# Kernel tuning notes

Hardware: AMD Instinct MI355X
Metric: run time of the kernel (lower is better)

## Reference

```python
import jax, jax.numpy as jnp
import numpy as np

N_NODES = 30000
N_EDGES = 480000
N_GRAPHS = 128
D_IN = 128
D_H = 256
N_CLASSES = 60


def gcn_conv(x, src, dst, norm, W, b, num_nodes):
    # x: [N, d_in]; W: [d_out, d_in]; b: [d_out]
    h = x @ W.T                                   # [N, d_out]
    msg = h[src] * norm[:, None]                  # [E+N, d_out] gather + scale
    out = jax.ops.segment_sum(msg, dst, num_segments=num_nodes)  # scatter-add
    return out + b


def setup_inputs() -> dict:
    key = jax.random.key(0)
    ks = jax.random.split(key, 10)
    glorot = lambda k, o, i: jax.random.normal(k, (o, i), jnp.float32) * (2.0 / (o + i)) ** 0.5
    x = jax.random.normal(ks[0], (N_NODES, D_IN), jnp.float32)
    edge_index = jax.random.randint(ks[1], (2, N_EDGES), 0, N_NODES, jnp.int64)
    batch = jnp.sort(jax.random.randint(ks[2], (N_NODES,), 0, N_GRAPHS, jnp.int64))
    return {
        "x": x,
        "edge_index": edge_index,
        "batch": batch,
        "W1": glorot(ks[3], D_H, D_IN), "b1": jnp.zeros((D_H,), jnp.float32),
        "W2": glorot(ks[4], D_H, D_H),  "b2": jnp.zeros((D_H,), jnp.float32),
        "W3": glorot(ks[5], D_H, D_H),  "b3": jnp.zeros((D_H,), jnp.float32),
        "Wfc": glorot(ks[6], N_CLASSES, D_H),
        "bfc": jnp.zeros((N_CLASSES,), jnp.float32),
    }


def reference(x, edge_index, batch, W1, b1, W2, b2, W3, b3, Wfc, bfc):
    num_nodes = x.shape[0]
    # GCNConv default: add self-loops, symmetric normalization D^-1/2 A D^-1/2
    loops = jnp.arange(num_nodes, dtype=edge_index.dtype)
    src = jnp.concatenate([edge_index[0], loops])
    dst = jnp.concatenate([edge_index[1], loops])
    deg = jax.ops.segment_sum(jnp.ones_like(dst, dtype=x.dtype), dst,
                              num_segments=num_nodes)
    dinv = jnp.where(deg > 0, jax.lax.rsqrt(deg), 0.0)
    norm = dinv[src] * dinv[dst]                  # per-edge normalization

    h = jax.nn.relu(gcn_conv(x, src, dst, norm, W1, b1, num_nodes))
    h = jax.nn.relu(gcn_conv(h, src, dst, norm, W2, b2, num_nodes))
    h = jax.nn.relu(gcn_conv(h, src, dst, norm, W3, b3, num_nodes))

    # global_mean_pool over graph ids
    sums = jax.ops.segment_sum(h, batch, num_segments=N_GRAPHS)
    cnts = jax.ops.segment_sum(jnp.ones((num_nodes,), h.dtype), batch,
                               num_segments=N_GRAPHS)
    pooled = sums / jnp.maximum(cnts, 1.0)[:, None]   # [G, 256]
    return pooled @ Wfc.T + bfc                       # [G, num_classes]
```

## Files before the change

kernel.cpp:

```cpp
#include <hip/hip_runtime.h>
#include <cstdint>
#include <cstddef>

#define NN 30000
#define NE 480000
#define NG 128
#define DIN 128
#define DH 256
#define NC 60
#define CAP 64
#define P1MAX (NN * DIN / 4)

typedef _Float16 f16x8 __attribute__((ext_vector_type(8)));
typedef _Float16 half4_t __attribute__((ext_vector_type(4)));
typedef float f32x4 __attribute__((ext_vector_type(4)));

__device__ __forceinline__ void gload_lds16(const _Float16* g, _Float16* l) {
    __builtin_amdgcn_global_load_lds(
        (const __attribute__((address_space(1))) void*)g,
        (__attribute__((address_space(3))) void*)l, 16, 0, 0);
}

__global__ __launch_bounds__(256) void k_pre(const int* __restrict__ ei, int* __restrict__ cursor,
        int* __restrict__ csr_src,
        const float* __restrict__ x, _Float16* __restrict__ xh,
        const float* __restrict__ W1, const float* __restrict__ W2, const float* __restrict__ W3,
        _Float16* __restrict__ w1h, _Float16* __restrict__ w2h, _Float16* __restrict__ w3h,
        float* __restrict__ sums) {
    int i = blockIdx.x * 256 + threadIdx.x;
    if (i < NE) {
        int s = ei[i];
        int d = ei[NE + i];
        int slot = atomicAdd(&cursor[d], 1);
        if (slot < CAP) csr_src[d * CAP + slot] = s;
    }
    if (i < P1MAX) {
        float4 v = ((const float4*)x)[i];
        half4_t o;
        o[0] = (_Float16)v.x; o[1] = (_Float16)v.y;
        o[2] = (_Float16)v.z; o[3] = (_Float16)v.w;
        ((half4_t*)xh)[i] = o;
    }
    if (i < DH * DIN) w1h[i] = (_Float16)W1[i];
    if (i < DH * DH) {
        w2h[i] = (_Float16)W2[i];
        w3h[i] = (_Float16)W3[i];
    }
    if (i < NG * DH) sums[i] = 0.f;
}

template<int K>
__global__ __launch_bounds__(256) void k_agg(const _Float16* __restrict__ hin,
        _Float16* __restrict__ tout, const int* __restrict__ cnt,
        const int* __restrict__ csr_src) {
    constexpr int L = K / 8;
    constexpr int G = 64 / L;
    constexpr int B16 = 16 / G;
    constexpr int B8 = 8 / G;
    int node = blockIdx.x * 4 + (threadIdx.x >> 6);
    int lane = threadIdx.x & 63;
    int sub = lane / L;
    int off = lane % L;
    const _Float16* gbase = hin + off * 8;
    float acc[8];
    #pragma unroll
    for (int u = 0; u < 8; u++) acc[u] = 0.f;
    int deg = cnt[node];
    float dvd = rsqrtf((float)(deg + 1));
    int c = deg < CAP ? deg : CAP;
    int beg = node * CAP, end = beg + c;
    int e = beg;
    for (; e + 16 <= end; e += 16) {
        int s[B16]; float w[B16]; f16x8 r[B16];
        #pragma unroll
        for (int j = 0; j < B16; j++) s[j] = csr_src[e + j * G + sub];
        #pragma unroll
        for (int j = 0; j < B16; j++) r[j] = *(const f16x8*)(gbase + (size_t)s[j] * K);
        #pragma unroll
        for (int j = 0; j < B16; j++) w[j] = rsqrtf((float)(cnt[s[j]] + 1)) * dvd;
        #pragma unroll
        for (int j = 0; j < B16; j++)
            #pragma unroll
            for (int u = 0; u < 8; u++) acc[u] = fmaf(w[j], (float)r[j][u], acc[u]);
    }
    for (; e < end; e += 8) {
        int s[B8]; float w[B8]; f16x8 r[B8];
        #pragma unroll
        for (int j = 0; j < B8; j++) {
            int idx = e + j * G + sub;
            s[j] = (idx < end) ? csr_src[idx] : node;
        }
        #pragma unroll
        for (int j = 0; j < B8; j++)
            r[j] = *(const f16x8*)(gbase + (size_t)s[j] * K);
        #pragma unroll
        for (int j = 0; j < B8; j++) {
            int idx = e + j * G + sub;
            w[j] = (idx < end) ? rsqrtf((float)(cnt[s[j]] + 1)) * dvd : 0.f;
        }
        #pragma unroll
        for (int j = 0; j < B8; j++)
            #pragma unroll
            for (int u = 0; u < 8; u++) acc[u] = fmaf(w[j], (float)r[j][u], acc[u]);
    }
    {
        float sws = (sub == 0) ? dvd * dvd : 0.f;
        f16x8 rs = *(const f16x8*)(gbase + (size_t)node * K);
        #pragma unroll
        for (int u = 0; u < 8; u++) acc[u] = fmaf(sws, (float)rs[u], acc[u]);
    }
    #pragma unroll
    for (int u = 0; u < 8; u++) {
        float v = acc[u];
        #pragma unroll
        for (int m = L; m < 64; m <<= 1) v += __shfl_xor(v, m, 64);
        acc[u] = v;
    }
    if (sub == 0) {
        f16x8 o;
        #pragma unroll
        for (int u = 0; u < 8; u++) o[u] = (_Float16)acc[u];
        *(f16x8*)(tout + (size_t)node * K + off * 8) = o;
    }
}

template<int K, bool FUSE_POOL>
__global__ __launch_bounds__(256, 8) void k_gemm(const _Float16* __restrict__ A,
        const _Float16* __restrict__ W, const float* __restrict__ bias,
        _Float16* __restrict__ Cb, const int* __restrict__ batch,
        float* __restrict__ sums) {
    __shared__ __align__(16) _Float16 lsA[64 * 64];
    __shared__ __align__(16) _Float16 lsB[64 * 64];
    int t = threadIdx.x;
    int bm = blockIdx.x * 64;
    int bn = blockIdx.y * 64;
    int lane = t & 63, wv = t >> 6;
    int wm = (wv & 1) * 32;
    int wn = (wv >> 1) * 32;
    int lm = lane & 15, q = lane >> 4;
    int r8 = t >> 3;
    int cs = t & 7;
    int c0 = (cs ^ (r8 & 7)) * 8;
    int ra0 = bm + r8;      if (ra0 >= NN) ra0 = NN - 1;
    int ra1 = bm + 32 + r8; if (ra1 >= NN) ra1 = NN - 1;
    int rb0 = bn + r8;
    int rb1 = bn + 32 + r8;
    const _Float16* gA0 = A + (size_t)ra0 * K + c0;
    const _Float16* gA1 = A + (size_t)ra1 * K + c0;
    const _Float16* gW0 = W + (size_t)rb0 * K + c0;
    const _Float16* gW1 = W + (size_t)rb1 * K + c0;
    _Float16* dA = lsA + t * 8;
    _Float16* dW = lsB + t * 8;

    f32x4 acc[2][2];
    #pragma unroll
    for (int i = 0; i < 2; i++)
        #pragma unroll
        for (int j = 0; j < 2; j++) acc[i][j] = (f32x4){0.f, 0.f, 0.f, 0.f};

    for (int k0 = 0; k0 < K; k0 += 64) {
        __syncthreads();
        gload_lds16(gA0 + k0, dA);
        gload_lds16(gA1 + k0, dA + 2048);
        gload_lds16(gW0 + k0, dW);
        gload_lds16(gW1 + k0, dW + 2048);
        __syncthreads();
        #pragma unroll
        for (int kk = 0; kk < 2; kk++) {
            f16x8 bf[2], af[2];
            #pragma unroll
            for (int nt = 0; nt < 2; nt++) {
                int row = wn + nt * 16 + lm;
                bf[nt] = *(const f16x8*)&lsB[row * 64 + (((kk * 4 + q) ^ (row & 7)) * 8)];
            }
            #pragma unroll
            for (int mt = 0; mt < 2; mt++) {
                int row = wm + mt * 16 + lm;
                af[mt] = *(const f16x8*)&lsA[row * 64 + (((kk * 4 + q) ^ (row & 7)) * 8)];
            }
            #pragma unroll
            for (int mt = 0; mt < 2; mt++)
                #pragma unroll
                for (int nt = 0; nt < 2; nt++)
                    acc[mt][nt] = __builtin_amdgcn_mfma_f32_16x16x32_f16(af[mt], bf[nt], acc[mt][nt], 0, 0, 0);
        }
    }
    if constexpr (!FUSE_POOL) {
        __syncthreads();
        #pragma unroll
        for (int mt = 0; mt < 2; mt++) {
            #pragma unroll
            for (int nt = 0; nt < 2; nt++) {
                int col = wn + nt * 16 + lm;
                float bv = bias[bn + col];
                #pragma unroll
                for (int r = 0; r < 4; r++) {
                    int row = wm + mt * 16 + q * 4 + r;
                    lsA[row * 64 + col] = (_Float16)fmaxf(acc[mt][nt][r] + bv, 0.f);
                }
            }
        }
        __syncthreads();
        int lr = t >> 3, lc = (t & 7) * 8;
        f16x8 v0 = *(const f16x8*)&lsA[lr * 64 + lc];
        f16x8 v1 = *(const f16x8*)&lsA[(lr + 32) * 64 + lc];
        int orow0 = bm + lr, orow1 = bm + 32 + lr;
        if (orow0 < NN) *(f16x8*)&Cb[(size_t)orow0 * 256 + bn + lc] = v0;
        if (orow1 < NN) *(f16x8*)&Cb[(size_t)orow1 * 256 + bn + lc] = v1;
    } else {
        int gid[8];
        #pragma unroll
        for (int mt = 0; mt < 2; mt++)
            #pragma unroll
            for (int r = 0; r < 4; r++) {
                int row = bm + wm + mt * 16 + q * 4 + r;
                gid[mt * 4 + r] = (row < NN) ? batch[row] : -1;
            }
        #pragma unroll
        for (int nt = 0; nt < 2; nt++) {
            int col = bn + wn + nt * 16 + lm;
            float bv = bias[col];
            float runsum = 0.f;
            int curg = -1;
            #pragma unroll
            for (int mt = 0; mt < 2; mt++) {
                #pragma unroll
                for (int r = 0; r < 4; r++) {
                    int g = gid[mt * 4 + r];
                    if (g >= 0) {
                        float v = fmaxf(acc[mt][nt][r] + bv, 0.f);
                        if (g != curg) {
                            if (curg >= 0) atomicAdd(&sums[curg * DH + col], runsum);
                            curg = g;
                            runsum = 0.f;
                        }
                        runsum += v;
                    }
                }
            }
            if (curg >= 0) atomicAdd(&sums[curg * DH + col], runsum);
        }
    }
}

__global__ __launch_bounds__(64) void k_fc(const float* __restrict__ sums,
        const int* __restrict__ batch, const float* __restrict__ Wfc,
        const float* __restrict__ bfc, float* __restrict__ out) {
    __shared__ float p[DH];
    int g = blockIdx.x;
    int t = threadIdx.x;
    int lo = 0, hi = NN;
    while (lo < hi) { int mid = (lo + hi) >> 1; if (batch[mid] < g) lo = mid + 1; else hi = mid; }
    int start = lo;
    hi = NN;
    while (lo < hi) { int mid = (lo + hi) >> 1; if (batch[mid] < g + 1) lo = mid + 1; else hi = mid; }
    int cnt = lo - start;
    float inv = (cnt > 0) ? 1.f / (float)cnt : 0.f;
    for (int i = t; i < DH; i += 64) p[i] = sums[g * DH + i] * inv;
    __syncthreads();
    if (t < NC) {
        float a = bfc[t];
        for (int k = 0; k < DH; k++) a = fmaf(p[k], Wfc[t * DH + k], a);
        out[g * NC + t] = a;
    }
}

extern "C" void kernel_launch(void* const* d_in, const int* in_sizes, int n_in,
                              void* d_out, int out_size, void* d_ws, size_t ws_size,
                              hipStream_t stream) {
    const float* x     = (const float*)d_in[0];
    const int*   ei    = (const int*)d_in[1];
    const int*   batch = (const int*)d_in[2];
    const float* W1 = (const float*)d_in[3];
    const float* b1 = (const float*)d_in[4];
    const float* W2 = (const float*)d_in[5];
    const float* b2 = (const float*)d_in[6];
    const float* W3 = (const float*)d_in[7];
    const float* b3 = (const float*)d_in[8];
    const float* Wfc = (const float*)d_in[9];
    const float* bfc = (const float*)d_in[10];
    float* out = (float*)d_out;

    char* wp = (char*)d_ws;
    auto alloc = [&](size_t bytes) {
        char* q = wp;
        wp += (bytes + 511) & ~(size_t)511;
        return (void*)q;
    };
    int*   cursor  = (int*)alloc((size_t)NN * 4);
    int*   csr_src = (int*)alloc((size_t)NN * CAP * 4);
    float* sums    = (float*)alloc((size_t)NG * DH * 4);
    _Float16* xh   = (_Float16*)alloc((size_t)NN * DIN * 2);
    _Float16* tb   = (_Float16*)alloc((size_t)NN * DH * 2);
    _Float16* hA   = (_Float16*)alloc((size_t)NN * DH * 2);
    _Float16* hB   = (_Float16*)alloc((size_t)NN * DH * 2);
    _Float16* w1h = (_Float16*)alloc((size_t)DH * DIN * 2);
    _Float16* w2h = (_Float16*)alloc((size_t)DH * DH * 2);
    _Float16* w3h = (_Float16*)alloc((size_t)DH * DH * 2);

    hipMemsetAsync(cursor, 0, (size_t)NN * 4, stream);

    k_pre<<<(P1MAX + 255) / 256, 256, 0, stream>>>(ei, cursor, csr_src, x, xh,
                                                   W1, W2, W3, w1h, w2h, w3h, sums);

    dim3 gg((NN + 63) / 64, 4);
    k_agg<128><<<NN / 4, 256, 0, stream>>>(xh, tb, cursor, csr_src);
    k_gemm<128, false><<<gg, 256, 0, stream>>>(tb, w1h, b1, hA, nullptr, nullptr);
    k_agg<256><<<NN / 4, 256, 0, stream>>>(hA, tb, cursor, csr_src);
    k_gemm<256, false><<<gg, 256, 0, stream>>>(tb, w2h, b2, hB, nullptr, nullptr);
    k_agg<256><<<NN / 4, 256, 0, stream>>>(hB, tb, cursor, csr_src);
    k_gemm<256, true><<<gg, 256, 0, stream>>>(tb, w3h, b3, nullptr, batch, sums);

    k_fc<<<NG, 64, 0, stream>>>(sums, batch, Wfc, bfc, out);
}
```

Measured before the change: 268.6 us.

## Map multiple nodes per wavefront in aggregation, removing cross-lane reductions

The aggregation kernel now gives each group of L lanes (one per 8-feature chunk) its own destination node, so a wavefront handles 64/L nodes instead of splitting one node's edges across lane groups. Each lane walks all of its node's edges sequentially, which removes the shuffle-based reduction and the sub==0 predicated store. Grid sizes shrink to match. In exchange each lane issues more sequential gathers per node, and lanes in a wave see different degrees, which adds divergence and load imbalance.

```diff
diff --git a/kernel.cpp b/kernel.cpp
--- a/kernel.cpp
+++ b/kernel.cpp
@@ -54,12 +54,10 @@
         _Float16* __restrict__ tout, const int* __restrict__ cnt,
         const int* __restrict__ csr_src) {
     constexpr int L = K / 8;
-    constexpr int G = 64 / L;
-    constexpr int B16 = 16 / G;
-    constexpr int B8 = 8 / G;
-    int node = blockIdx.x * 4 + (threadIdx.x >> 6);
+    constexpr int NW = 64 / L;
+    constexpr int NB = NW * 4;
     int lane = threadIdx.x & 63;
-    int sub = lane / L;
+    int node = blockIdx.x * NB + (threadIdx.x >> 6) * NW + lane / L;
     int off = lane % L;
     const _Float16* gbase = hin + off * 8;
     float acc[8];
@@ -71,57 +69,48 @@
     int beg = node * CAP, end = beg + c;
     int e = beg;
     for (; e + 16 <= end; e += 16) {
-        int s[B16]; float w[B16]; f16x8 r[B16];
-        #pragma unroll
-        for (int j = 0; j < B16; j++) s[j] = csr_src[e + j * G + sub];
-        #pragma unroll
-        for (int j = 0; j < B16; j++) r[j] = *(const f16x8*)(gbase + (size_t)s[j] * K);
-        #pragma unroll
-        for (int j = 0; j < B16; j++) w[j] = rsqrtf((float)(cnt[s[j]] + 1)) * dvd;
-        #pragma unroll
-        for (int j = 0; j < B16; j++)
+        int s[16]; float w[16]; f16x8 r[16];
+        #pragma unroll
+        for (int j = 0; j < 16; j++) s[j] = csr_src[e + j];
+        #pragma unroll
+        for (int j = 0; j < 16; j++) r[j] = *(const f16x8*)(gbase + (size_t)s[j] * K);
+        #pragma unroll
+        for (int j = 0; j < 16; j++) w[j] = rsqrtf((float)(cnt[s[j]] + 1)) * dvd;
+        #pragma unroll
+        for (int j = 0; j < 16; j++)
             #pragma unroll
             for (int u = 0; u < 8; u++) acc[u] = fmaf(w[j], (float)r[j][u], acc[u]);
     }
     for (; e < end; e += 8) {
-        int s[B8]; float w[B8]; f16x8 r[B8];
-        #pragma unroll
-        for (int j = 0; j < B8; j++) {
-            int idx = e + j * G + sub;
+        int s[8]; float w[8]; f16x8 r[8];
+        #pragma unroll
+        for (int j = 0; j < 8; j++) {
+            int idx = e + j;
             s[j] = (idx < end) ? csr_src[idx] : node;
         }
         #pragma unroll
-        for (int j = 0; j < B8; j++)
+        for (int j = 0; j < 8; j++)
             r[j] = *(const f16x8*)(gbase + (size_t)s[j] * K);
         #pragma unroll
-        for (int j = 0; j < B8; j++) {
-            int idx = e + j * G + sub;
+        for (int j = 0; j < 8; j++) {
+            int idx = e + j;
             w[j] = (idx < end) ? rsqrtf((float)(cnt[s[j]] + 1)) * dvd : 0.f;
         }
         #pragma unroll
-        for (int j = 0; j < B8; j++)
+        for (int j = 0; j < 8; j++)
             #pragma unroll
             for (int u = 0; u < 8; u++) acc[u] = fmaf(w[j], (float)r[j][u], acc[u]);
     }
     {
-        float sws = (sub == 0) ? dvd * dvd : 0.f;
+        float sws = dvd * dvd;
         f16x8 rs = *(const f16x8*)(gbase + (size_t)node * K);
         #pragma unroll
         for (int u = 0; u < 8; u++) acc[u] = fmaf(sws, (float)rs[u], acc[u]);
     }
+    f16x8 o;
     #pragma unroll
-    for (int u = 0; u < 8; u++) {
-        float v = acc[u];
-        #pragma unroll
-        for (int m = L; m < 64; m <<= 1) v += __shfl_xor(v, m, 64);
-        acc[u] = v;
-    }
-    if (sub == 0) {
-        f16x8 o;
-        #pragma unroll
-        for (int u = 0; u < 8; u++) o[u] = (_Float16)acc[u];
-        *(f16x8*)(tout + (size_t)node * K + off * 8) = o;
-    }
+    for (int u = 0; u < 8; u++) o[u] = (_Float16)acc[u];
+    *(f16x8*)(tout + (size_t)node * K + off * 8) = o;
 }
 
 template<int K, bool FUSE_POOL>
@@ -304,11 +293,11 @@
                                                    W1, W2, W3, w1h, w2h, w3h, sums);
 
     dim3 gg((NN + 63) / 64, 4);
-    k_agg<128><<<NN / 4, 256, 0, stream>>>(xh, tb, cursor, csr_src);
+    k_agg<128><<<NN / 16, 256, 0, stream>>>(xh, tb, cursor, csr_src);
     k_gemm<128, false><<<gg, 256, 0, stream>>>(tb, w1h, b1, hA, nullptr, nullptr);
-    k_agg<256><<<NN / 4, 256, 0, stream>>>(hA, tb, cursor, csr_src);
+    k_agg<256><<<NN / 8, 256, 0, stream>>>(hA, tb, cursor, csr_src);
     k_gemm<256, false><<<gg, 256, 0, stream>>>(tb, w2h, b2, hB, nullptr, nullptr);
-    k_agg<256><<<NN / 4, 256, 0, stream>>>(hB, tb, cursor, csr_src);
+    k_agg<256><<<NN / 8, 256, 0, stream>>>(hB, tb, cursor, csr_src);
     k_gemm<256, true><<<gg, 256, 0, stream>>>(tb, w3h, b3, nullptr, batch, sums);
 
     k_fc<<<NG, 64, 0, stream>>>(sums, batch, Wfc, bfc, out);
```

New measurement: 285.2 us. 6.2% more time.
